# Kernel optimization log

Measured on AMD Instinct MI355X. Metric: run time of the kernel, lower is better.

## Reference

```python
import jax, jax.numpy as jnp
import numpy as np

PATCH_SIZE = 50        # hardcoded in forward (overrides __init__ args)
NUM_PATCHES_OUT = 50   # size of the weighted_x buffer
TOPK = 4


def setup_inputs() -> dict:
    key = jax.random.key(0)
    k1, k2 = jax.random.split(key)
    x = jax.random.normal(k1, (1024, 12, 2500), dtype=jnp.float32)
    # self.weights = sigmoid(sample from N(0,1)) -> a scalar in (0,1)
    weights = jax.nn.sigmoid(jax.random.normal(k2, (), dtype=jnp.float32))
    return {"x": x, "weights": weights}


def reference(x, weights):
    B, N, L = x.shape
    # power spectrum |FFT(x)|^2 along time axis
    power = jnp.abs(jnp.fft.fft(x, axis=2)) ** 2            # [B,N,L] f32
    _, idx = jax.lax.top_k(power, TOPK)                      # [B,N,K] descending
    # only lead 0 and topk positions {0, 2} are used by the original code
    idx2 = idx[:, 0, ::2]                                    # [B,2] int32
    # np.fft.fftfreq(L)[i] = i/L for i <= (L-1)//2 else (i-L)/L
    k_signed = jnp.where(idx2 <= (L - 1) // 2, idx2, idx2 - L)
    valid = k_signed != 0                                    # freq == 0 -> skip
    # ideal_peak_interval = int(|1/freq|) = L // |k| (exact integer math)
    period = L // jnp.maximum(jnp.abs(k_signed), 1)          # [B,2] >= 2
    P = L // PATCH_SIZE                                      # effective num_patches
    starts = jnp.arange(P, dtype=jnp.int32) * PATCH_SIZE     # [P]
    # patch [start, start+PATCH_SIZE) contains a peak (multiple of period)
    # iff the first multiple >= start is < start + PATCH_SIZE
    p = period[..., None]                                    # [B,2,1]
    first_mult = ((starts[None, None, :] + p - 1) // p) * p  # [B,2,P]
    hit = (first_mult < starts[None, None, :] + PATCH_SIZE) & valid[..., None]
    counts = hit.sum(axis=1)                                 # [B,P] in {0,1,2}
    # the b/n loops add `weights` N times per (b, patch, freq-slot) hit
    weighted = (N * weights) * counts.astype(jnp.float32)    # [B,P]
    out = jnp.zeros((B, NUM_PATCHES_OUT), jnp.float32).at[:, :P].set(weighted)
    # original detaches via a numpy round-trip -> no gradient flows
    return jax.lax.stop_gradient(out)
```

## Files before the change

kernel.cpp:

```cpp
#include <hip/hip_runtime.h>

typedef _Float16 f16;
typedef _Float16 f16x4 __attribute__((ext_vector_type(4)));
typedef _Float16 f16x8 __attribute__((ext_vector_type(8)));
typedef float f32x4 __attribute__((ext_vector_type(4)));

#define L_N 2500
#define B_N 1024
#define ROWSTRIDE 30000
#define NPATCH 50
#define PATCH 50
#define KP 2560
#define NB 2560
#define ZSPLIT 4
#define KS_PER_Z 20

#define TWOPI_F 6.28318530717958647692f
#define RAD_PER_PH (6.283185307179586476925286766559 / 2500.0)

#define OFF_XH 0
#define SZ_XH (B_N * KP * 2)
#define OFF_W  (OFF_XH + SZ_XH)
#define SZ_W   (NB * KP * 2)
#define OFF_C  (OFF_W + SZ_W)
#define SZ_C   (B_N * NB * 4)

#define GLOAD16(gp, lp) __builtin_amdgcn_global_load_lds( \
    (const __attribute__((address_space(1))) unsigned int*)(gp), \
    (__attribute__((address_space(3))) unsigned int*)(lp), 16, 0, 0)

__global__ __launch_bounds__(256)
void gen_x(const float* __restrict__ x, f16* __restrict__ Xh) {
    const int row = blockIdx.x, tid = threadIdx.x;
#pragma unroll
    for (int i = 0; i < 3; ++i) {
        int slot = tid + 256 * i;
        if (slot < 640) {
            float4 v = make_float4(0.f, 0.f, 0.f, 0.f);
            if (slot < 625)
                v = *reinterpret_cast<const float4*>(x + (size_t)row * ROWSTRIDE + slot * 4);
            f16x4 h = { (f16)v.x, (f16)v.y, (f16)v.z, (f16)v.w };
            *reinterpret_cast<f16x4*>(Xh + (size_t)row * KP + slot * 4) = h;
        }
    }
}

__global__ __launch_bounds__(256)
void gen_w(f16* __restrict__ W) {
    const int bin = blockIdx.x;
    const int tid = threadIdx.x;
    for (int t = tid; t < KP; t += 256) {
        float c = 0.f, s = 0.f;
        if (t < L_N) {
            int ph = (bin * t) % L_N;
            float th = (float)ph * (TWOPI_F / (float)L_N);
            __sincosf(th, &s, &c);
        }
        W[(size_t)(2 * bin) * KP + t]     = (f16)c;
        W[(size_t)(2 * bin + 1) * KP + t] = (f16)s;
    }
}

__global__ void zero_c(float4* __restrict__ C) {
    int i = blockIdx.x * blockDim.x + threadIdx.x;
    C[i] = make_float4(0.f, 0.f, 0.f, 0.f);
}

__global__ __launch_bounds__(256)
void gemm_f16(const f16* __restrict__ A, const f16* __restrict__ W, float* __restrict__ C) {
    __shared__ f16 As[128 * 32];
    __shared__ f16 Bs[128 * 32];
    const int tid = threadIdx.x;
    const int wv = tid >> 6, lane = tid & 63;
    const int bm = blockIdx.x, bn = blockIdx.y;
    const int ks0 = blockIdx.z * KS_PER_Z;
    const int wr = wv >> 1, wc = wv & 1;
    const int lrow = lane & 15, lseg = lane >> 4;

    f32x4 acc[4][4];
#pragma unroll
    for (int m = 0; m < 4; ++m)
#pragma unroll
        for (int n = 0; n < 4; ++n) acc[m][n] = (f32x4){0.f, 0.f, 0.f, 0.f};

    const int c0 = wv * 128 + lane, c1 = c0 + 64;
    const int R0 = c0 >> 2, S0 = (c0 & 3) ^ ((R0 >> 1) & 3);
    const int R1 = c1 >> 2, S1 = (c1 & 3) ^ ((R1 >> 1) & 3);
    const f16* ga0 = A + (size_t)(bm * 128 + R0) * KP + S0 * 8;
    const f16* ga1 = A + (size_t)(bm * 128 + R1) * KP + S1 * 8;
    const f16* gb0 = W + (size_t)(bn * 128 + R0) * KP + S0 * 8;
    const f16* gb1 = W + (size_t)(bn * 128 + R1) * KP + S1 * 8;

    int aoff[4], boff[4];
#pragma unroll
    for (int m = 0; m < 4; ++m) {
        int ra = wr * 64 + m * 16 + lrow;
        aoff[m] = ra * 32 + ((lseg ^ ((ra >> 1) & 3)) * 8);
        int rb = wc * 64 + m * 16 + lrow;
        boff[m] = rb * 32 + ((lseg ^ ((rb >> 1) & 3)) * 8);
    }

    for (int ks = ks0; ks < ks0 + KS_PER_Z; ++ks) {
        const int kof = ks * 32;
        __syncthreads();
        GLOAD16(ga0 + kof, &As[c0 * 8]);
        GLOAD16(ga1 + kof, &As[c1 * 8]);
        GLOAD16(gb0 + kof, &Bs[c0 * 8]);
        GLOAD16(gb1 + kof, &Bs[c1 * 8]);
        __syncthreads();
        f16x8 af[4], bf[4];
#pragma unroll
        for (int m = 0; m < 4; ++m) af[m] = *(const f16x8*)&As[aoff[m]];
#pragma unroll
        for (int n = 0; n < 4; ++n) bf[n] = *(const f16x8*)&Bs[boff[n]];
#pragma unroll
        for (int m = 0; m < 4; ++m)
#pragma unroll
            for (int n = 0; n < 4; ++n)
                acc[m][n] = __builtin_amdgcn_mfma_f32_16x16x32_f16(af[m], bf[n], acc[m][n], 0, 0, 0);
    }
    const int orow0 = bm * 128 + wr * 64 + (lane >> 4) * 4;
    const int ocol0 = bn * 128 + wc * 64 + (lane & 15);
#pragma unroll
    for (int m = 0; m < 4; ++m)
#pragma unroll
        for (int n = 0; n < 4; ++n)
#pragma unroll
            for (int j = 0; j < 4; ++j)
                atomicAdd(&C[(size_t)(orow0 + m * 16 + j) * NB + ocol0 + n * 16], acc[m][n][j]);
}

__global__ __launch_bounds__(512)
void fused_sel(const float* __restrict__ x, const float* __restrict__ C,
               const float* __restrict__ wp, float* __restrict__ out) {
    __shared__ float xrow[KP];
    __shared__ unsigned long long keybuf[64];
    __shared__ int bins8s[8];
    __shared__ unsigned long long rk[8];
    const int row = blockIdx.x, tid = threadIdx.x;
    const int wv = tid >> 6, lane = tid & 63;

    for (int t = tid; t < KP; t += 512)
        xrow[t] = (t < L_N) ? x[(size_t)row * ROWSTRIDE + t] : 0.f;

    unsigned long long k3[3];
#pragma unroll
    for (int c = 0; c < 3; ++c) {
        int bin = tid + 512 * c;
        unsigned long long key = 0ULL;
        if (bin <= 1250) {
            float re = C[(size_t)row * NB + 2 * bin];
            float im = C[(size_t)row * NB + 2 * bin + 1];
            float p = re * re + im * im;
            key = ((unsigned long long)__float_as_uint(p) << 32) | (unsigned)(L_N - bin);
        }
        k3[c] = key;
    }
#pragma unroll
    for (int r = 0; r < 8; ++r) {
        unsigned long long m = k3[0];
        m = (k3[1] > m) ? k3[1] : m;
        m = (k3[2] > m) ? k3[2] : m;
#pragma unroll
        for (int off = 32; off > 0; off >>= 1) {
            unsigned long long o = __shfl_xor(m, off, 64);
            m = (o > m) ? o : m;
        }
        if (k3[0] == m) k3[0] = 0ULL;
        if (k3[1] == m) k3[1] = 0ULL;
        if (k3[2] == m) k3[2] = 0ULL;
        if (lane == 0) keybuf[wv * 8 + r] = m;
    }
    __syncthreads();
    if (wv == 0) {
        unsigned long long cur = keybuf[lane];
#pragma unroll
        for (int r = 0; r < 8; ++r) {
            unsigned long long m = cur;
#pragma unroll
            for (int off = 32; off > 0; off >>= 1) {
                unsigned long long o = __shfl_xor(m, off, 64);
                m = (o > m) ? o : m;
            }
            if (cur == m) cur = 0ULL;
            if (lane == 0) bins8s[r] = L_N - (int)(unsigned)(m & 0xffffffffULL);
        }
    }
    __syncthreads();

    const int k = bins8s[wv];
    double c, s, cd, sd;
    {
        int ph0 = (k * lane) % L_N;
        int phd = (k * 64) % L_N;
        sincos((double)ph0 * RAD_PER_PH, &s, &c);
        sincos((double)phd * RAD_PER_PH, &sd, &cd);
    }
    double re = 0.0, im = 0.0;
#pragma unroll 4
    for (int i = 0; i < 40; ++i) {
        double xv = (double)xrow[lane + 64 * i];
        re += xv * c;
        im += xv * s;
        double cn = c * cd - s * sd;
        double sn = s * cd + c * sd;
        c = cn; s = sn;
    }
#pragma unroll
    for (int off = 32; off > 0; off >>= 1) {
        re += __shfl_xor(re, off, 64);
        im += __shfl_xor(im, off, 64);
    }
    if (lane == 0) {
        double p = re * re + im * im;
        unsigned long long pb = (unsigned long long)__double_as_longlong(p);
        rk[wv] = (pb & ~2047ULL) | (unsigned long long)(1250 - k);
    }
    __syncthreads();

    if (tid < NPATCH) {
        unsigned long long q[8];
#pragma unroll
        for (int r = 0; r < 8; ++r) q[r] = rk[r];
        unsigned long long m1 = q[0];
#pragma unroll
        for (int r = 1; r < 8; ++r) m1 = (q[r] > m1) ? q[r] : m1;
#pragma unroll
        for (int r = 0; r < 8; ++r) if (q[r] == m1) q[r] = 0;
        unsigned long long m2 = q[0];
#pragma unroll
        for (int r = 1; r < 8; ++r) m2 = (q[r] > m2) ? q[r] : m2;
#pragma unroll
        for (int r = 0; r < 8; ++r) if (q[r] == m2) q[r] = 0;
        unsigned long long m3 = q[0];
#pragma unroll
        for (int r = 1; r < 8; ++r) m3 = (q[r] > m3) ? q[r] : m3;

        int kA = 1250 - (int)(m1 & 2047ULL);
        int kB = 1250 - (int)(m2 & 2047ULL);
        int kC = 1250 - (int)(m3 & 2047ULL);
        int multA = (kA == 0 || kA == 1250) ? 1 : 2;
        int multB = (kB == 0 || kB == 1250) ? 1 : 2;
        int sel0 = kA;
        int sel1 = (multA == 2 || multB == 2) ? kB : kC;

        int start = tid * PATCH;
        int cnt = 0;
        if (sel0 != 0) {
            int p = L_N / sel0;
            int fm = ((start + p - 1) / p) * p;
            if (fm < start + PATCH) ++cnt;
        }
        if (sel1 != 0) {
            int p = L_N / sel1;
            int fm = ((start + p - 1) / p) * p;
            if (fm < start + PATCH) ++cnt;
        }
        out[(size_t)row * NPATCH + tid] = 12.0f * wp[0] * (float)cnt;
    }
}

extern "C" void kernel_launch(void* const* d_in, const int* in_sizes, int n_in,
                              void* d_out, int out_size, void* d_ws, size_t ws_size,
                              hipStream_t stream) {
    const float* x = (const float*)d_in[0];
    const float* w = (const float*)d_in[1];
    float* out = (float*)d_out;
    char* ws = (char*)d_ws;

    f16* Xh = (f16*)(ws + OFF_XH);
    f16* W  = (f16*)(ws + OFF_W);
    float* C = (float*)(ws + OFF_C);

    gen_x<<<B_N, 256, 0, stream>>>(x, Xh);
    gen_w<<<1280, 256, 0, stream>>>(W);
    zero_c<<<SZ_C / 16 / 256, 256, 0, stream>>>((float4*)C);
    gemm_f16<<<dim3(8, 20, ZSPLIT), 256, 0, stream>>>(Xh, W, C);
    fused_sel<<<B_N, 512, 0, stream>>>(x, C, w, out);
}
```

Baseline: 235.5 us.

## Fuse prep kernels, double-buffer GEMM LDS loads, vectorize row loads

After: 228.5 us. 3.0% less time.

```diff
diff --git a/kernel.cpp b/kernel.cpp
--- a/kernel.cpp
+++ b/kernel.cpp
@@ -25,51 +25,54 @@
 #define OFF_C  (OFF_W + SZ_W)
 #define SZ_C   (B_N * NB * 4)
 
+#define PB_X    B_N
+#define PB_W    1280
+#define PB_Z    (SZ_C / 16 / 256)
+#define PB_TOT  (PB_X + PB_W + PB_Z)
+
 #define GLOAD16(gp, lp) __builtin_amdgcn_global_load_lds( \
     (const __attribute__((address_space(1))) unsigned int*)(gp), \
     (__attribute__((address_space(3))) unsigned int*)(lp), 16, 0, 0)
 
 __global__ __launch_bounds__(256)
-void gen_x(const float* __restrict__ x, f16* __restrict__ Xh) {
-    const int row = blockIdx.x, tid = threadIdx.x;
-#pragma unroll
-    for (int i = 0; i < 3; ++i) {
-        int slot = tid + 256 * i;
-        if (slot < 640) {
-            float4 v = make_float4(0.f, 0.f, 0.f, 0.f);
-            if (slot < 625)
-                v = *reinterpret_cast<const float4*>(x + (size_t)row * ROWSTRIDE + slot * 4);
-            f16x4 h = { (f16)v.x, (f16)v.y, (f16)v.z, (f16)v.w };
-            *reinterpret_cast<f16x4*>(Xh + (size_t)row * KP + slot * 4) = h;
-        }
-    }
-}
-
-__global__ __launch_bounds__(256)
-void gen_w(f16* __restrict__ W) {
-    const int bin = blockIdx.x;
-    const int tid = threadIdx.x;
-    for (int t = tid; t < KP; t += 256) {
-        float c = 0.f, s = 0.f;
-        if (t < L_N) {
-            int ph = (bin * t) % L_N;
-            float th = (float)ph * (TWOPI_F / (float)L_N);
-            __sincosf(th, &s, &c);
-        }
-        W[(size_t)(2 * bin) * KP + t]     = (f16)c;
-        W[(size_t)(2 * bin + 1) * KP + t] = (f16)s;
-    }
-}
-
-__global__ void zero_c(float4* __restrict__ C) {
-    int i = blockIdx.x * blockDim.x + threadIdx.x;
-    C[i] = make_float4(0.f, 0.f, 0.f, 0.f);
+void prep(const float* __restrict__ x, f16* __restrict__ Xh,
+          f16* __restrict__ W, float4* __restrict__ C4) {
+    const int b = blockIdx.x, tid = threadIdx.x;
+    if (b < PB_X) {
+        const int row = b;
+#pragma unroll
+        for (int i = 0; i < 3; ++i) {
+            int slot = tid + 256 * i;
+            if (slot < 640) {
+                float4 v = make_float4(0.f, 0.f, 0.f, 0.f);
+                if (slot < 625)
+                    v = *reinterpret_cast<const float4*>(x + (size_t)row * ROWSTRIDE + slot * 4);
+                f16x4 h = { (f16)v.x, (f16)v.y, (f16)v.z, (f16)v.w };
+                *reinterpret_cast<f16x4*>(Xh + (size_t)row * KP + slot * 4) = h;
+            }
+        }
+    } else if (b < PB_X + PB_W) {
+        const int bin = b - PB_X;
+        for (int t = tid; t < KP; t += 256) {
+            float c = 0.f, s = 0.f;
+            if (t < L_N) {
+                int ph = (bin * t) % L_N;
+                float th = (float)ph * (TWOPI_F / (float)L_N);
+                __sincosf(th, &s, &c);
+            }
+            W[(size_t)(2 * bin) * KP + t]     = (f16)c;
+            W[(size_t)(2 * bin + 1) * KP + t] = (f16)s;
+        }
+    } else {
+        int i = (b - PB_X - PB_W) * 256 + tid;
+        C4[i] = make_float4(0.f, 0.f, 0.f, 0.f);
+    }
 }
 
 __global__ __launch_bounds__(256)
 void gemm_f16(const f16* __restrict__ A, const f16* __restrict__ W, float* __restrict__ C) {
-    __shared__ f16 As[128 * 32];
-    __shared__ f16 Bs[128 * 32];
+    __shared__ f16 As[2][128 * 32];
+    __shared__ f16 Bs[2][128 * 32];
     const int tid = threadIdx.x;
     const int wv = tid >> 6, lane = tid & 63;
     const int bm = blockIdx.x, bn = blockIdx.y;
@@ -100,25 +103,39 @@
         boff[m] = rb * 32 + ((lseg ^ ((rb >> 1) & 3)) * 8);
     }
 
-    for (int ks = ks0; ks < ks0 + KS_PER_Z; ++ks) {
-        const int kof = ks * 32;
-        __syncthreads();
-        GLOAD16(ga0 + kof, &As[c0 * 8]);
-        GLOAD16(ga1 + kof, &As[c1 * 8]);
-        GLOAD16(gb0 + kof, &Bs[c0 * 8]);
-        GLOAD16(gb1 + kof, &Bs[c1 * 8]);
-        __syncthreads();
+    {
+        const int kof = ks0 * 32;
+        GLOAD16(ga0 + kof, &As[0][c0 * 8]);
+        GLOAD16(ga1 + kof, &As[0][c1 * 8]);
+        GLOAD16(gb0 + kof, &Bs[0][c0 * 8]);
+        GLOAD16(gb1 + kof, &Bs[0][c1 * 8]);
+    }
+    __syncthreads();
+
+    int cur = 0;
+    for (int t = 0; t < KS_PER_Z; ++t) {
+        const int nxt = cur ^ 1;
+        if (t + 1 < KS_PER_Z) {
+            const int kof = (ks0 + t + 1) * 32;
+            GLOAD16(ga0 + kof, &As[nxt][c0 * 8]);
+            GLOAD16(ga1 + kof, &As[nxt][c1 * 8]);
+            GLOAD16(gb0 + kof, &Bs[nxt][c0 * 8]);
+            GLOAD16(gb1 + kof, &Bs[nxt][c1 * 8]);
+        }
         f16x8 af[4], bf[4];
 #pragma unroll
-        for (int m = 0; m < 4; ++m) af[m] = *(const f16x8*)&As[aoff[m]];
-#pragma unroll
-        for (int n = 0; n < 4; ++n) bf[n] = *(const f16x8*)&Bs[boff[n]];
+        for (int m = 0; m < 4; ++m) af[m] = *(const f16x8*)&As[cur][aoff[m]];
+#pragma unroll
+        for (int n = 0; n < 4; ++n) bf[n] = *(const f16x8*)&Bs[cur][boff[n]];
 #pragma unroll
         for (int m = 0; m < 4; ++m)
 #pragma unroll
             for (int n = 0; n < 4; ++n)
                 acc[m][n] = __builtin_amdgcn_mfma_f32_16x16x32_f16(af[m], bf[n], acc[m][n], 0, 0, 0);
-    }
+        __syncthreads();
+        cur = nxt;
+    }
+
     const int orow0 = bm * 128 + wr * 64 + (lane >> 4) * 4;
     const int ocol0 = bn * 128 + wc * 64 + (lane & 15);
 #pragma unroll
@@ -140,8 +157,14 @@
     const int row = blockIdx.x, tid = threadIdx.x;
     const int wv = tid >> 6, lane = tid & 63;
 
-    for (int t = tid; t < KP; t += 512)
-        xrow[t] = (t < L_N) ? x[(size_t)row * ROWSTRIDE + t] : 0.f;
+    if (tid < 60) xrow[2500 + tid] = 0.f;
+#pragma unroll
+    for (int i = 0; i < 2; ++i) {
+        int slot = tid + 512 * i;
+        if (slot < 625)
+            *reinterpret_cast<float4*>(&xrow[slot * 4]) =
+                *reinterpret_cast<const float4*>(x + (size_t)row * ROWSTRIDE + slot * 4);
+    }
 
     unsigned long long k3[3];
 #pragma unroll
@@ -149,9 +172,8 @@
         int bin = tid + 512 * c;
         unsigned long long key = 0ULL;
         if (bin <= 1250) {
-            float re = C[(size_t)row * NB + 2 * bin];
-            float im = C[(size_t)row * NB + 2 * bin + 1];
-            float p = re * re + im * im;
+            float2 ri = *reinterpret_cast<const float2*>(&C[(size_t)row * NB + 2 * bin]);
+            float p = ri.x * ri.x + ri.y * ri.y;
             key = ((unsigned long long)__float_as_uint(p) << 32) | (unsigned)(L_N - bin);
         }
         k3[c] = key;
@@ -272,9 +294,7 @@
     f16* W  = (f16*)(ws + OFF_W);
     float* C = (float*)(ws + OFF_C);
 
-    gen_x<<<B_N, 256, 0, stream>>>(x, Xh);
-    gen_w<<<1280, 256, 0, stream>>>(W);
-    zero_c<<<SZ_C / 16 / 256, 256, 0, stream>>>((float4*)C);
+    prep<<<PB_TOT, 256, 0, stream>>>(x, Xh, W, (float4*)C);
     gemm_f16<<<dim3(8, 20, ZSPLIT), 256, 0, stream>>>(Xh, W, C);
     fused_sel<<<B_N, 512, 0, stream>>>(x, C, w, out);
 }
```
